# Kernel optimization log

Measured on AMD Instinct MI355X. Metric: run time of the kernel, lower is better.

## Reference

```python
import jax, jax.numpy as jnp
import numpy as np


def _l2_normalize(x, eps=1e-12):
    # matches torch F.normalize(p=2): x / max(||x||, eps)
    n = jnp.linalg.norm(x, axis=-1, keepdims=True)
    return x / jnp.maximum(n, eps)


def _linear_sum_assignment(cost):
    """Jonker-Volgenant shortest augmenting path (same optimum as scipy
    linear_sum_assignment) for a square cost matrix. Returns col4row:
    col4row[r] = column assigned to row r (minimization)."""
    n = cost.shape[0]
    INF = np.inf
    u = np.zeros(n + 1)
    v = np.zeros(n + 1)
    p = np.zeros(n + 1, dtype=np.int64)   # p[j] = row (1-based) assigned to col j
    way = np.zeros(n + 1, dtype=np.int64)
    for i in range(1, n + 1):
        p[0] = i
        j0 = 0
        minv = np.full(n + 1, INF)
        used = np.zeros(n + 1, dtype=bool)
        while True:
            used[j0] = True
            i0 = p[j0]
            cur = cost[i0 - 1] - u[i0] - v[1:]          # reduced costs of row i0
            free = ~used[1:]
            upd = free & (cur < minv[1:])
            idx = np.nonzero(upd)[0]
            minv[idx + 1] = cur[idx]
            way[idx + 1] = j0
            freeidx = np.nonzero(free)[0]
            jrel = freeidx[np.argmin(minv[freeidx + 1])]
            delta = minv[jrel + 1]
            u[p[used]] += delta
            v[used] -= delta
            minv[~used] -= delta
            j0 = jrel + 1
            if p[j0] == 0:
                break
        while j0:
            j1 = way[j0]
            p[j0] = p[j1]
            j0 = j1
    col4row = np.empty(n, dtype=np.int64)
    col4row[p[1:] - 1] = np.arange(n)
    return col4row


def setup_inputs() -> dict:
    key = jax.random.key(0)
    k1, k2 = jax.random.split(key)
    B, N, D = 128, 256, 64
    inputs = jax.random.normal(k1, (B, N, D), dtype=jnp.float32)
    targets = jax.random.normal(k2, (B, N, D), dtype=jnp.float32)
    return {"inputs": inputs, "targets": targets}


def reference(inputs, targets):
    ip = _l2_normalize(inputs)                     # [B, N, D]
    tg = _l2_normalize(targets)                    # [B, N, D]
    cos = jnp.einsum('bad,bcd->bac', ip, tg)       # [B, N, N]
    self_cos = jnp.einsum('bad,bcd->bac', ip, ip)  # [B, N, N]
    # strip the diagonal: tril(-1)[:, :-1] + triu(1)[:, 1:] -> [B, N, N-1]
    self_off = jnp.tril(self_cos, k=-1)[:, :, :-1] + jnp.triu(self_cos, k=1)[:, :, 1:]
    # Hungarian assignment on host (non-differentiable, as in the torch code)
    cost = np.asarray(jax.lax.stop_gradient(-cos))
    tgt = jnp.asarray(np.stack([_linear_sum_assignment(cost[b]) for b in range(cost.shape[0])]))  # [B, N]
    logits = jnp.concatenate([cos, self_off], axis=-1)        # [B, N, 2N-1]
    logp = jax.nn.log_softmax(logits, axis=-1)
    nll = -jnp.take_along_axis(logp, tgt[..., None], axis=-1)[..., 0]  # [B, N]
    # per-sample cross_entropy is mean over N; batch_loss / B -> global mean
    return jnp.mean(nll)
```

## Files before the change

kernel.cpp:

```cpp
#include <hip/hip_runtime.h>
#include <math.h>

#define BB 128
#define NN 256
#define DD 64
constexpr int NROWS = BB * NN;

__global__ __launch_bounds__(256) void norm_kernel(const float* __restrict__ inp,
                                                   const float* __restrict__ tgin,
                                                   float* __restrict__ ipn,
                                                   float* __restrict__ tgn) {
  int wid = threadIdx.x >> 6;
  int lane = threadIdx.x & 63;
  int row = blockIdx.x * 4 + wid;
  const float* src;
  float* dst;
  int r = row;
  if (row < NROWS) { src = inp; dst = ipn; }
  else { src = tgin; dst = tgn; r = row - NROWS; }
  float x = src[(size_t)r * DD + lane];
  float s = x * x;
  #pragma unroll
  for (int off = 32; off; off >>= 1) s += __shfl_xor(s, off);
  float nrm = sqrtf(s);
  float scale = 1.0f / fmaxf(nrm, 1e-12f);
  dst[(size_t)r * DD + lane] = x * scale;
}

__global__ __launch_bounds__(256) void gemm_kernel(const float* __restrict__ ipn,
                                                   const float* __restrict__ tgn,
                                                   float* __restrict__ cosm,
                                                   float* __restrict__ selfm) {
  __shared__ float As[64 * 64];
  __shared__ float Bs[64 * 64];
  int b = blockIdx.y;
  int ti = (blockIdx.x >> 2) * 64;
  int tj = (blockIdx.x & 3) * 64;
  const float* A = ipn + (size_t)b * NN * DD + (size_t)ti * DD;
  const float* Bm = (blockIdx.z ? ipn : tgn) + (size_t)b * NN * DD + (size_t)tj * DD;
  float* Out = (blockIdx.z ? selfm : cosm) + (size_t)b * NN * NN;
  int t = threadIdx.x;
  #pragma unroll
  for (int i = 0; i < 4; ++i) {
    int f4 = t + 256 * i;
    int row = f4 >> 4;
    int k0 = (f4 & 15) << 2;
    float4 a = reinterpret_cast<const float4*>(A)[f4];
    float4 v = reinterpret_cast<const float4*>(Bm)[f4];
    As[(k0 + 0) * 64 + row] = a.x; As[(k0 + 1) * 64 + row] = a.y;
    As[(k0 + 2) * 64 + row] = a.z; As[(k0 + 3) * 64 + row] = a.w;
    Bs[(k0 + 0) * 64 + row] = v.x; Bs[(k0 + 1) * 64 + row] = v.y;
    Bs[(k0 + 2) * 64 + row] = v.z; Bs[(k0 + 3) * 64 + row] = v.w;
  }
  __syncthreads();
  int tx = t & 15, ty = t >> 4;
  float acc[4][4] = {};
  #pragma unroll 8
  for (int k = 0; k < 64; ++k) {
    float4 av = *reinterpret_cast<const float4*>(&As[k * 64 + ty * 4]);
    float4 bv = *reinterpret_cast<const float4*>(&Bs[k * 64 + tx * 4]);
    float ar[4] = {av.x, av.y, av.z, av.w};
    float br[4] = {bv.x, bv.y, bv.z, bv.w};
    #pragma unroll
    for (int r = 0; r < 4; ++r)
      #pragma unroll
      for (int c = 0; c < 4; ++c)
        acc[r][c] = fmaf(ar[r], br[c], acc[r][c]);
  }
  #pragma unroll
  for (int r = 0; r < 4; ++r) {
    float4 o = {acc[r][0], acc[r][1], acc[r][2], acc[r][3]};
    *reinterpret_cast<float4*>(&Out[(size_t)(ti + ty * 4 + r) * NN + tj + tx * 4]) = o;
  }
}

__device__ __forceinline__ int sel4i(const int a[4], int q) {
  int r = a[0];
  if (q == 1) r = a[1];
  else if (q == 2) r = a[2];
  else if (q == 3) r = a[3];
  return r;
}
__device__ __forceinline__ void set4i(int a[4], int q, int v) {
  if (q == 0) a[0] = v;
  else if (q == 1) a[1] = v;
  else if (q == 2) a[2] = v;
  else a[3] = v;
}
__device__ __forceinline__ int readlane_i(int x, int l) {
  return __builtin_amdgcn_readlane(x, l);
}
__device__ __forceinline__ unsigned wave_min_u32(unsigned x) {
  unsigned t;
  #define DPP_STEP(ctrl)                                                        \
    t = (unsigned)__builtin_amdgcn_update_dpp((int)x, (int)x, ctrl, 0xF, 0xF,   \
                                              false);                           \
    x = (t < x) ? t : x;
  DPP_STEP(0x111)
  DPP_STEP(0x112)
  DPP_STEP(0x114)
  DPP_STEP(0x118)
  DPP_STEP(0x142)
  DPP_STEP(0x143)
  #undef DPP_STEP
  return x;
}

__global__ __launch_bounds__(64) void hungarian_kernel(const float* __restrict__ cosm,
                                                       int* __restrict__ tgt) {
  const int b = blockIdx.x;
  const float* __restrict__ C = cosm + (size_t)b * NN * NN;
  __shared__ unsigned short Cs[NN * NN];
  __shared__ int u_lds[NN];
  const int lane = threadIdx.x;
  const int col0 = lane * 4;

  const float4* Cf4 = reinterpret_cast<const float4*>(C);
  #pragma unroll 4
  for (int it = 0; it < NN * NN / 4 / 64; ++it) {
    float4 f = Cf4[it * 64 + lane];
    unsigned u0 = __float2uint_rn(fmaxf(32768.f - f.x * 32768.f, 0.f));
    unsigned u1 = __float2uint_rn(fmaxf(32768.f - f.y * 32768.f, 0.f));
    unsigned u2 = __float2uint_rn(fmaxf(32768.f - f.z * 32768.f, 0.f));
    unsigned u3 = __float2uint_rn(fmaxf(32768.f - f.w * 32768.f, 0.f));
    u0 = u0 > 65535u ? 65535u : u0;
    u1 = u1 > 65535u ? 65535u : u1;
    u2 = u2 > 65535u ? 65535u : u2;
    u3 = u3 > 65535u ? 65535u : u3;
    uint2 packed;
    packed.x = u0 | (u1 << 16);
    packed.y = u2 | (u3 << 16);
    *reinterpret_cast<uint2*>(&Cs[(it * 64 + lane) * 4]) = packed;
  }
  #pragma unroll
  for (int q = 0; q < 4; ++q) u_lds[col0 + q] = 0;

  int vv[4];
  #pragma unroll
  for (int q = 0; q < 4; ++q) vv[q] = col0 + q;
  int p[4] = {0, 0, 0, 0};

  for (int i = 1; i <= NN; ++i) {
    unsigned key[4] = {0xFFFFFFFFu, 0xFFFFFFFFu, 0xFFFFFFFFu, 0xFFFFFFFFu};
    int way[4] = {-1, -1, -1, -1};
    int usedm = 0;
    int Delta = 0;
    int j0 = -1;
    int u_i0 = 0;
    int row = i - 1;
    uint2 raw = *reinterpret_cast<const uint2*>(&Cs[(size_t)row * NN + col0]);
    int jf;

    while (true) {
      int t0s8 = (Delta - u_i0) << 8;
      int cs[4];
      cs[0] = (int)((raw.x & 0xFFFFu) << 8);
      cs[1] = (int)((raw.x >> 8) & 0x00FFFF00u);
      cs[2] = (int)((raw.y & 0xFFFFu) << 8);
      cs[3] = (int)((raw.y >> 8) & 0x00FFFF00u);
      #pragma unroll
      for (int q = 0; q < 4; ++q) {
        unsigned nk = (unsigned)(t0s8 + cs[q] + vv[q]);
        if (nk < key[q]) { key[q] = nk; way[q] = j0; }
      }
      unsigned c0 = (usedm & 1) ? 0xFFFFFFFFu : key[0];
      unsigned c1 = (usedm & 2) ? 0xFFFFFFFFu : key[1];
      unsigned c2 = (usedm & 4) ? 0xFFFFFFFFu : key[2];
      unsigned c3 = (usedm & 8) ? 0xFFFFFFFFu : key[3];
      unsigned loc = c0 < c1 ? c0 : c1;
      unsigned l2 = c2 < c3 ? c2 : c3;
      loc = loc < l2 ? loc : l2;
      unsigned K = (unsigned)readlane_i((int)wave_min_u32(loc), 63);
      int j1 = (int)(K & 0xFFu);
      Delta = (int)(K >> 8);
      int pnext = readlane_i(sel4i(p, j1 & 3), j1 >> 2);
      if (pnext == 0) { jf = j1; break; }
      row = pnext - 1;
      raw = *reinterpret_cast<const uint2*>(&Cs[(size_t)row * NN + col0]);
      u_i0 = u_lds[row];
      if (lane == (j1 >> 2)) usedm |= 1 << (j1 & 3);
      j0 = j1;
    }

    #pragma unroll
    for (int q = 0; q < 4; ++q) {
      if ((usedm >> q) & 1) {
        int dd = Delta - (int)(key[q] >> 8);
        vv[q] += dd << 8;
        u_lds[p[q] - 1] += dd;
      }
    }
    if (lane == 0) u_lds[i - 1] = Delta;

    int j = jf;
    while (true) {
      int w = readlane_i(sel4i(way, j & 3), j >> 2);
      int newv;
      if (w < 0) newv = i;
      else newv = readlane_i(sel4i(p, w & 3), w >> 2);
      if (lane == (j >> 2)) set4i(p, j & 3, newv);
      if (w < 0) break;
      j = w;
    }
  }
  #pragma unroll
  for (int q = 0; q < 4; ++q)
    tgt[(size_t)b * NN + (p[q] - 1)] = col0 + q;
}

__global__ __launch_bounds__(256) void nll_kernel(const float* __restrict__ cosm,
                                                  const float* __restrict__ selfm,
                                                  const int* __restrict__ tgt,
                                                  float* __restrict__ nll) {
  int lane = threadIdx.x & 63, wid = threadIdx.x >> 6;
  int row = blockIdx.x * 4 + wid;
  int r = row & (NN - 1);
  const float* crow = cosm + (size_t)row * NN;
  const float* srow = selfm + (size_t)row * NN;
  float xc[4], xs[4];
  float m = -INFINITY;
  #pragma unroll
  for (int q = 0; q < 4; ++q) {
    int j = lane + 64 * q;
    xc[q] = crow[j];
    xs[q] = (j == r) ? -INFINITY : srow[j];
    m = fmaxf(m, fmaxf(xc[q], xs[q]));
  }
  #pragma unroll
  for (int off = 32; off; off >>= 1) m = fmaxf(m, __shfl_xor(m, off));
  float s = 0.f;
  #pragma unroll
  for (int q = 0; q < 4; ++q) {
    s += expf(xc[q] - m);
    s += (xs[q] == -INFINITY) ? 0.f : expf(xs[q] - m);
  }
  #pragma unroll
  for (int off = 32; off; off >>= 1) s += __shfl_xor(s, off);
  if (lane == 0) {
    float lse = m + logf(s);
    nll[row] = lse - crow[tgt[row]];
  }
}

__global__ __launch_bounds__(256) void reduce_kernel(const float* __restrict__ nll,
                                                     float* __restrict__ out) {
  __shared__ float sm[256];
  int t = threadIdx.x;
  float s = 0.f;
  for (int i = t; i < NROWS; i += 256) s += nll[i];
  sm[t] = s;
  __syncthreads();
  for (int st = 128; st; st >>= 1) {
    if (t < st) sm[t] += sm[t + st];
    __syncthreads();
  }
  if (t == 0) out[0] = sm[0] / (float)NROWS;
}

extern "C" void kernel_launch(void* const* d_in, const int* in_sizes, int n_in,
                              void* d_out, int out_size, void* d_ws, size_t ws_size,
                              hipStream_t stream) {
  const float* inputs = (const float*)d_in[0];
  const float* targets = (const float*)d_in[1];
  float* ws = (float*)d_ws;
  float* ipn = ws;
  float* tgn = ipn + (size_t)BB * NN * DD;
  float* cosm = tgn + (size_t)BB * NN * DD;
  float* selfm = cosm + (size_t)BB * NN * NN;
  int* tgt = (int*)(selfm + (size_t)BB * NN * NN);
  float* nll = (float*)(tgt + BB * NN);

  norm_kernel<<<2 * NROWS / 4, 256, 0, stream>>>(inputs, targets, ipn, tgn);
  gemm_kernel<<<dim3(16, BB, 2), 256, 0, stream>>>(ipn, tgn, cosm, selfm);
  hungarian_kernel<<<BB, 64, 0, stream>>>(cosm, tgt);
  nll_kernel<<<NROWS / 4, 256, 0, stream>>>(cosm, selfm, tgt, nll);
  reduce_kernel<<<1, 256, 0, stream>>>(nll, (float*)d_out);
}
```

Before: 1.283 ms.

## Add JV column reduction and augmenting row reduction before shortest-path phase

Adds the Jonker-Volgenant initialization to the Hungarian kernel. Column reduction assigns each column's minimum row, with atomicMax resolving conflicts. An auction-style augmenting row reduction pass over the compacted free rows then settles most assignments cheaply and derives the duals u from v. Only the rows still free then run the expensive shortest-augmenting-path loop. This should cut the number of serial Dijkstra iterations, at the cost of extra LDS arrays and an iteration-capped heuristic phase that must keep the duals consistent for an optimal result.

Result: slower. 2.729 ms (+112.8%).

```diff
diff --git a/kernel.cpp b/kernel.cpp
--- a/kernel.cpp
+++ b/kernel.cpp
@@ -105,6 +105,24 @@
   #undef DPP_STEP
   return x;
 }
+__device__ __forceinline__ int compact_free(const int* x_lds, int* Fl, int lane) {
+  int row0 = lane * 4;
+  int4 xv = *reinterpret_cast<const int4*>(&x_lds[row0]);
+  int f0 = (xv.x < 0), f1 = (xv.y < 0), f2 = (xv.z < 0), f3 = (xv.w < 0);
+  int cnt = f0 + f1 + f2 + f3;
+  int sc = cnt;
+  #pragma unroll
+  for (int off = 1; off < 64; off <<= 1) {
+    int t = __shfl_up(sc, off);
+    if (lane >= off) sc += t;
+  }
+  int pos = sc - cnt;
+  if (f0) { Fl[pos] = row0 + 0; pos++; }
+  if (f1) { Fl[pos] = row0 + 1; pos++; }
+  if (f2) { Fl[pos] = row0 + 2; pos++; }
+  if (f3) { Fl[pos] = row0 + 3; pos++; }
+  return readlane_i(sc, 63);
+}
 
 __global__ __launch_bounds__(64) void hungarian_kernel(const float* __restrict__ cosm,
                                                        int* __restrict__ tgt) {
@@ -112,6 +130,9 @@
   const float* __restrict__ C = cosm + (size_t)b * NN * NN;
   __shared__ unsigned short Cs[NN * NN];
   __shared__ int u_lds[NN];
+  __shared__ int x_lds[NN];
+  __shared__ int claim[NN];
+  __shared__ int Fl[1024];
   const int lane = threadIdx.x;
   const int col0 = lane * 4;
 
@@ -132,15 +153,118 @@
     packed.y = u2 | (u3 << 16);
     *reinterpret_cast<uint2*>(&Cs[(it * 64 + lane) * 4]) = packed;
   }
-  #pragma unroll
-  for (int q = 0; q < 4; ++q) u_lds[col0 + q] = 0;
-
+  {
+    int4 mi = {-1, -1, -1, -1};
+    *reinterpret_cast<int4*>(&x_lds[col0]) = mi;
+    *reinterpret_cast<int4*>(&claim[col0]) = mi;
+  }
+
+  int m0 = 0x7FFFFFFF, m1 = 0x7FFFFFFF, m2 = 0x7FFFFFFF, m3 = 0x7FFFFFFF;
+  int a0 = 0, a1 = 0, a2 = 0, a3 = 0;
+  #pragma unroll 4
+  for (int i = 0; i < NN; ++i) {
+    uint2 raw = *reinterpret_cast<const uint2*>(&Cs[(size_t)i * NN + col0]);
+    int c0 = (int)(raw.x & 0xFFFFu), c1 = (int)(raw.x >> 16);
+    int c2 = (int)(raw.y & 0xFFFFu), c3 = (int)(raw.y >> 16);
+    if (c0 < m0) { m0 = c0; a0 = i; }
+    if (c1 < m1) { m1 = c1; a1 = i; }
+    if (c2 < m2) { m2 = c2; a2 = i; }
+    if (c3 < m3) { m3 = c3; a3 = i; }
+  }
+  atomicMax(&claim[a0], col0 + 0);
+  atomicMax(&claim[a1], col0 + 1);
+  atomicMax(&claim[a2], col0 + 2);
+  atomicMax(&claim[a3], col0 + 3);
+  int p[4];
   int vv[4];
-  #pragma unroll
-  for (int q = 0; q < 4; ++q) vv[q] = col0 + q;
-  int p[4] = {0, 0, 0, 0};
-
-  for (int i = 1; i <= NN; ++i) {
+  p[0] = (claim[a0] == col0 + 0) ? a0 + 1 : 0;
+  p[1] = (claim[a1] == col0 + 1) ? a1 + 1 : 0;
+  p[2] = (claim[a2] == col0 + 2) ? a2 + 1 : 0;
+  p[3] = (claim[a3] == col0 + 3) ? a3 + 1 : 0;
+  if (p[0]) x_lds[a0] = col0 + 0;
+  if (p[1]) x_lds[a1] = col0 + 1;
+  if (p[2]) x_lds[a2] = col0 + 2;
+  if (p[3]) x_lds[a3] = col0 + 3;
+  vv[0] = (col0 + 0) - (m0 << 8);
+  vv[1] = (col0 + 1) - (m1 << 8);
+  vv[2] = (col0 + 2) - (m2 << 8);
+  vv[3] = (col0 + 3) - (m3 << 8);
+
+  {
+    int cnt = compact_free(x_lds, Fl, lane);
+    int k = 0, steps = 0;
+    while (k < cnt && steps < 4096) {
+      ++steps;
+      int i = Fl[k]; ++k;
+      uint2 raw = *reinterpret_cast<const uint2*>(&Cs[(size_t)i * NN + col0]);
+      unsigned key[4];
+      key[0] = (unsigned)((int)((raw.x & 0xFFFFu) << 8) + vv[0]);
+      key[1] = (unsigned)((int)((raw.x >> 8) & 0x00FFFF00u) + vv[1]);
+      key[2] = (unsigned)((int)((raw.y & 0xFFFFu) << 8) + vv[2]);
+      key[3] = (unsigned)((int)((raw.y >> 8) & 0x00FFFF00u) + vv[3]);
+      unsigned lo01 = key[0] < key[1] ? key[0] : key[1];
+      unsigned lo23 = key[2] < key[3] ? key[2] : key[3];
+      unsigned loc = lo01 < lo23 ? lo01 : lo23;
+      unsigned K1 = (unsigned)readlane_i((int)wave_min_u32(loc), 63);
+      int j1 = (int)(K1 & 0xFFu);
+      if (lane == (j1 >> 2)) {
+        int qq = j1 & 3;
+        if (qq == 0) key[0] = 0xFFFFFFFFu;
+        else if (qq == 1) key[1] = 0xFFFFFFFFu;
+        else if (qq == 2) key[2] = 0xFFFFFFFFu;
+        else key[3] = 0xFFFFFFFFu;
+      }
+      lo01 = key[0] < key[1] ? key[0] : key[1];
+      lo23 = key[2] < key[3] ? key[2] : key[3];
+      loc = lo01 < lo23 ? lo01 : lo23;
+      unsigned K2 = (unsigned)readlane_i((int)wave_min_u32(loc), 63);
+      unsigned u1v = K1 >> 8, u2v = K2 >> 8;
+      bool lower = u1v < u2v;
+      int owner1 = readlane_i(sel4i(p, j1 & 3), j1 >> 2) - 1;
+      int jf, i0;
+      if (lower) {
+        int dq = (int)(u2v - u1v) << 8;
+        if (lane == (j1 >> 2)) {
+          int qq = j1 & 3;
+          if (qq == 0) vv[0] += dq;
+          else if (qq == 1) vv[1] += dq;
+          else if (qq == 2) vv[2] += dq;
+          else vv[3] += dq;
+        }
+        jf = j1; i0 = owner1;
+      } else if (owner1 >= 0) {
+        jf = (int)(K2 & 0xFFu);
+        i0 = readlane_i(sel4i(p, jf & 3), jf >> 2) - 1;
+      } else {
+        jf = j1; i0 = -1;
+      }
+      if (lane == (jf >> 2)) set4i(p, jf & 3, i + 1);
+      if (lane == 0) {
+        x_lds[i] = jf;
+        if (i0 >= 0) x_lds[i0] = -1;
+      }
+      if (i0 >= 0) {
+        if (lower) { --k; if (lane == 0) Fl[k] = i0; }
+        else if (cnt < 1024) { if (lane == 0) Fl[cnt] = i0; ++cnt; }
+      }
+    }
+  }
+
+  claim[col0 + 0] = ((col0 + 0) - vv[0]) >> 8;
+  claim[col0 + 1] = ((col0 + 1) - vv[1]) >> 8;
+  claim[col0 + 2] = ((col0 + 2) - vv[2]) >> 8;
+  claim[col0 + 3] = ((col0 + 3) - vv[3]) >> 8;
+  {
+    int4 xr = *reinterpret_cast<const int4*>(&x_lds[col0]);
+    u_lds[col0 + 0] = (xr.x >= 0) ? ((int)Cs[(size_t)(col0 + 0) * NN + xr.x] - claim[xr.x]) : 0;
+    u_lds[col0 + 1] = (xr.y >= 0) ? ((int)Cs[(size_t)(col0 + 1) * NN + xr.y] - claim[xr.y]) : 0;
+    u_lds[col0 + 2] = (xr.z >= 0) ? ((int)Cs[(size_t)(col0 + 2) * NN + xr.z] - claim[xr.z]) : 0;
+    u_lds[col0 + 3] = (xr.w >= 0) ? ((int)Cs[(size_t)(col0 + 3) * NN + xr.w] - claim[xr.w]) : 0;
+  }
+  int nfree = compact_free(x_lds, Fl, lane);
+
+  for (int idx = 0; idx < nfree; ++idx) {
+    int i = Fl[idx] + 1;
     unsigned key[4] = {0xFFFFFFFFu, 0xFFFFFFFFu, 0xFFFFFFFFu, 0xFFFFFFFFu};
     int way[4] = {-1, -1, -1, -1};
     int usedm = 0;
```

## Warm-start Hungarian with column-reduction initial assignment and free-row compaction

Applied to the files above, without the earlier changes.

Adds a Jonker-Volgenant style column reduction: each column finds its minimum-cost row, sets the dual v to that minimum, and uncontested rows are assigned directly. Only the remaining free rows, compacted with a wave prefix scan, go through the shortest augmenting path loop. This is meant to cut the number of serial augmentation iterations per batch. It adds an initial pass over the cost matrix in LDS plus atomics, and depends on the duals staying feasible with the quantized costs.

After: 1.207 ms. 1.06x faster.

```diff
diff --git a/kernel.cpp b/kernel.cpp
--- a/kernel.cpp
+++ b/kernel.cpp
@@ -105,6 +105,24 @@
   #undef DPP_STEP
   return x;
 }
+__device__ __forceinline__ int compact_free(const int* x_lds, int* Fl, int lane) {
+  int row0 = lane * 4;
+  int4 xv = *reinterpret_cast<const int4*>(&x_lds[row0]);
+  int f0 = (xv.x < 0), f1 = (xv.y < 0), f2 = (xv.z < 0), f3 = (xv.w < 0);
+  int cnt = f0 + f1 + f2 + f3;
+  int sc = cnt;
+  #pragma unroll
+  for (int off = 1; off < 64; off <<= 1) {
+    int t = __shfl_up(sc, off);
+    if (lane >= off) sc += t;
+  }
+  int pos = sc - cnt;
+  if (f0) { Fl[pos] = row0 + 0; pos++; }
+  if (f1) { Fl[pos] = row0 + 1; pos++; }
+  if (f2) { Fl[pos] = row0 + 2; pos++; }
+  if (f3) { Fl[pos] = row0 + 3; pos++; }
+  return readlane_i(sc, 63);
+}
 
 __global__ __launch_bounds__(64) void hungarian_kernel(const float* __restrict__ cosm,
                                                        int* __restrict__ tgt) {
@@ -112,6 +130,9 @@
   const float* __restrict__ C = cosm + (size_t)b * NN * NN;
   __shared__ unsigned short Cs[NN * NN];
   __shared__ int u_lds[NN];
+  __shared__ int x_lds[NN];
+  __shared__ int claim[NN];
+  __shared__ int Fl[NN];
   const int lane = threadIdx.x;
   const int col0 = lane * 4;
 
@@ -132,15 +153,49 @@
     packed.y = u2 | (u3 << 16);
     *reinterpret_cast<uint2*>(&Cs[(it * 64 + lane) * 4]) = packed;
   }
-  #pragma unroll
-  for (int q = 0; q < 4; ++q) u_lds[col0 + q] = 0;
-
+  {
+    int4 mi = {-1, -1, -1, -1};
+    int4 zi = {0, 0, 0, 0};
+    *reinterpret_cast<int4*>(&x_lds[col0]) = mi;
+    *reinterpret_cast<int4*>(&claim[col0]) = mi;
+    *reinterpret_cast<int4*>(&u_lds[col0]) = zi;
+  }
+
+  int m0 = 0x7FFFFFFF, m1 = 0x7FFFFFFF, m2 = 0x7FFFFFFF, m3 = 0x7FFFFFFF;
+  int a0 = 0, a1 = 0, a2 = 0, a3 = 0;
+  #pragma unroll 4
+  for (int i = 0; i < NN; ++i) {
+    uint2 raw = *reinterpret_cast<const uint2*>(&Cs[(size_t)i * NN + col0]);
+    int c0 = (int)(raw.x & 0xFFFFu), c1 = (int)(raw.x >> 16);
+    int c2 = (int)(raw.y & 0xFFFFu), c3 = (int)(raw.y >> 16);
+    if (c0 < m0) { m0 = c0; a0 = i; }
+    if (c1 < m1) { m1 = c1; a1 = i; }
+    if (c2 < m2) { m2 = c2; a2 = i; }
+    if (c3 < m3) { m3 = c3; a3 = i; }
+  }
+  atomicMax(&claim[a0], col0 + 0);
+  atomicMax(&claim[a1], col0 + 1);
+  atomicMax(&claim[a2], col0 + 2);
+  atomicMax(&claim[a3], col0 + 3);
+  int p[4];
   int vv[4];
-  #pragma unroll
-  for (int q = 0; q < 4; ++q) vv[q] = col0 + q;
-  int p[4] = {0, 0, 0, 0};
-
-  for (int i = 1; i <= NN; ++i) {
+  p[0] = (claim[a0] == col0 + 0) ? a0 + 1 : 0;
+  p[1] = (claim[a1] == col0 + 1) ? a1 + 1 : 0;
+  p[2] = (claim[a2] == col0 + 2) ? a2 + 1 : 0;
+  p[3] = (claim[a3] == col0 + 3) ? a3 + 1 : 0;
+  if (p[0]) x_lds[a0] = col0 + 0;
+  if (p[1]) x_lds[a1] = col0 + 1;
+  if (p[2]) x_lds[a2] = col0 + 2;
+  if (p[3]) x_lds[a3] = col0 + 3;
+  vv[0] = (col0 + 0) - (m0 << 8);
+  vv[1] = (col0 + 1) - (m1 << 8);
+  vv[2] = (col0 + 2) - (m2 << 8);
+  vv[3] = (col0 + 3) - (m3 << 8);
+
+  int nfree = compact_free(x_lds, Fl, lane);
+
+  for (int idx = 0; idx < nfree; ++idx) {
+    int i = Fl[idx] + 1;
     unsigned key[4] = {0xFFFFFFFFu, 0xFFFFFFFFu, 0xFFFFFFFFu, 0xFFFFFFFFu};
     int way[4] = {-1, -1, -1, -1};
     int usedm = 0;
```
